# Optimization experiments

Hardware: AMD Instinct MI355X
Metric: run time of the kernel (lower is better)

The kernel has to match this reference:

```python
import jax, jax.numpy as jnp
import numpy as np

B, S, D = 4, 4096, 1024
H, W = 16, 256
DH = D // H


def setup_inputs() -> dict:
    key = jax.random.key(0)
    ks = jax.random.split(key, 5)
    sc = 1.0 / np.sqrt(D)
    return {
        "x": jax.random.normal(ks[0], (B, S, D), jnp.float32),
        "Wq": jax.random.normal(ks[1], (D, D), jnp.float32) * sc,
        "bq": jnp.zeros((D,), jnp.float32),
        "Wk": jax.random.normal(ks[2], (D, D), jnp.float32) * sc,
        "bk": jnp.zeros((D,), jnp.float32),
        "Wv": jax.random.normal(ks[3], (D, D), jnp.float32) * sc,
        "bv": jnp.zeros((D,), jnp.float32),
        "Wo": jax.random.normal(ks[4], (D, D), jnp.float32) * sc,
        "bo": jnp.zeros((D,), jnp.float32),
    }


def reference(x, Wq, bq, Wk, bk, Wv, bv, Wo, bo):
    b, s, d = x.shape
    n = s // W  # seq divisible by window_size -> no padding

    def split_heads(t):
        # (b, s, d) -> (b, h, n, w, dh)
        return t.reshape(b, n, W, H, DH).transpose(0, 3, 1, 2, 4)

    q = split_heads(x @ Wq + bq)
    k = split_heads(x @ Wk + bk)
    v = split_heads(x @ Wv + bv)

    scores = jnp.einsum("bhnqd,bhnkd->bhnqk", q, k) / jnp.sqrt(
        jnp.asarray(DH, x.dtype)
    )
    causal = jnp.tril(jnp.ones((W, W), bool))  # per-block causal mask
    neg = jnp.finfo(scores.dtype).min
    scores = jnp.where(causal, scores, neg)
    weights = jax.nn.softmax(scores, axis=-1)
    out = jnp.einsum("bhnqk,bhnkd->bhnqd", weights, v)
    # (b, h, n, w, dh) -> (b, s, d)
    out = out.transpose(0, 2, 3, 1, 4).reshape(b, s, d)
    return out @ Wo + bo
```

## Files before the change

kernel.cpp:

```cpp
#include <hip/hip_runtime.h>
#include <hip/hip_bf16.h>


typedef __attribute__((ext_vector_type(4))) float f32x4;
typedef __attribute__((ext_vector_type(8))) short s16x8;
typedef __attribute__((ext_vector_type(4))) short s16x4;

__device__ __forceinline__ short f2bf(float f) {
  unsigned u = __float_as_uint(f);
  u += 0x7fffu + ((u >> 16) & 1u);
  return (short)(u >> 16);
}

__device__ __forceinline__ void gload_lds16(const void* g, void* l) {
  __builtin_amdgcn_global_load_lds((const __attribute__((address_space(1))) void*)g,
                                   (__attribute__((address_space(3))) void*)l,
                                   16, 0, 0);
}

__device__ __forceinline__ float rmax16(float v) {
  v = fmaxf(v, __shfl_xor(v, 1, 64));
  v = fmaxf(v, __shfl_xor(v, 2, 64));
  v = fmaxf(v, __shfl_xor(v, 4, 64));
  v = fmaxf(v, __shfl_xor(v, 8, 64));
  return v;
}
__device__ __forceinline__ float rsum16(float v) {
  v += __shfl_xor(v, 1, 64);
  v += __shfl_xor(v, 2, 64);
  v += __shfl_xor(v, 4, 64);
  v += __shfl_xor(v, 8, 64);
  return v;
}

__global__ void cvt_x(const float4* __restrict__ in, s16x4* __restrict__ out, int n4) {
  for (int i = blockIdx.x * 256 + threadIdx.x; i < n4; i += gridDim.x * 256) {
    float4 v = in[i];
    s16x4 o;
    o[0] = f2bf(v.x); o[1] = f2bf(v.y); o[2] = f2bf(v.z); o[3] = f2bf(v.w);
    out[i] = o;
  }
}

__global__ void cvt_wT(const float* __restrict__ W0, const float* __restrict__ W1,
                       const float* __restrict__ W2, const float* __restrict__ W3,
                       short* __restrict__ out) {
  __shared__ float tile[64][65];
  const float* W = (blockIdx.y == 0) ? W0 : (blockIdx.y == 1) ? W1 : (blockIdx.y == 2) ? W2 : W3;
  short* o = out + (size_t)blockIdx.y * (1024 * 1024);
  const int kt = (blockIdx.x >> 4) << 6, nt = (blockIdx.x & 15) << 6;
  const int tid = threadIdx.x;
#pragma unroll
  for (int i = 0; i < 16; ++i) {
    int lin = i * 256 + tid;
    int r = lin >> 6, c = lin & 63;
    tile[r][c] = W[(size_t)(kt + r) * 1024 + nt + c];
  }
  __syncthreads();
#pragma unroll
  for (int i = 0; i < 16; ++i) {
    int lin = i * 256 + tid;
    int r = lin >> 6, c = lin & 63;
    o[(size_t)(nt + r) * 1024 + kt + c] = f2bf(tile[c][r]);
  }
}

template <int MODE>
__global__ __launch_bounds__(256) void gemm_bf16(const short* __restrict__ A,
                                                 const short* __restrict__ Bt,
                                                 const float* __restrict__ bias,
                                                 void* __restrict__ outp) {
  constexpr int Kd = 1024;
  __shared__ short As[128 * 32];
  __shared__ short Bs[128 * 32];
  const int tid = threadIdx.x;
  const int w = tid >> 6, lane = tid & 63;
  const int bm = blockIdx.x >> 3, bn = blockIdx.x & 7;
  const int m0 = bm << 7, n0 = bn << 7;
  const int wr = (w >> 1) << 6, wc = (w & 1) << 6;
  const int srow = lane >> 2, scol = (lane & 3) << 3;
  const int fr = lane & 15, fk = (lane >> 4) << 3;

  f32x4 acc[4][4];
#pragma unroll
  for (int i = 0; i < 4; ++i)
#pragma unroll
    for (int j = 0; j < 4; ++j) acc[i][j] = (f32x4){0.f, 0.f, 0.f, 0.f};

  for (int k0 = 0; k0 < Kd; k0 += 32) {
    __syncthreads();
#pragma unroll
    for (int i = 0; i < 2; ++i) {
      const int rr = ((i * 4 + w) << 4) + srow;
      gload_lds16(A + (size_t)(m0 + rr) * Kd + k0 + scol, As + ((i * 4 + w) << 9));
      gload_lds16(Bt + (size_t)(n0 + rr) * Kd + k0 + scol, Bs + ((i * 4 + w) << 9));
    }
    __syncthreads();
    s16x8 af[4], bf[4];
#pragma unroll
    for (int mi = 0; mi < 4; ++mi) af[mi] = *(const s16x8*)&As[(wr + mi * 16 + fr) * 32 + fk];
#pragma unroll
    for (int ni = 0; ni < 4; ++ni) bf[ni] = *(const s16x8*)&Bs[(wc + ni * 16 + fr) * 32 + fk];
#pragma unroll
    for (int mi = 0; mi < 4; ++mi)
#pragma unroll
      for (int ni = 0; ni < 4; ++ni)
        acc[mi][ni] = __builtin_amdgcn_mfma_f32_16x16x32_bf16(af[mi], bf[ni], acc[mi][ni], 0, 0, 0);
  }

  const int col0 = n0 + wc + fr;
  const int row0 = m0 + wr + ((lane >> 4) << 2);
#pragma unroll
  for (int mi = 0; mi < 4; ++mi) {
#pragma unroll
    for (int ni = 0; ni < 4; ++ni) {
      const int c = col0 + ni * 16;
      const float bv = bias[c];
#pragma unroll
      for (int jj = 0; jj < 4; ++jj) {
        const int r = row0 + mi * 16 + jj;
        const float v = acc[mi][ni][jj] + bv;
        if (MODE == 2) {
          ((float*)outp)[(size_t)r * 1024 + c] = v;
        } else {
          const int b = r >> 12, s = r & 4095;
          const int h = c >> 6, dh = c & 63;
          size_t addr;
          if (MODE == 0) addr = ((size_t)(b * 16 + h) * 4096 + s) * 64 + dh;
          else           addr = ((size_t)(b * 16 + h) * 64 + dh) * 4096 + s;
          ((short*)outp)[addr] = f2bf(v);
        }
      }
    }
  }
}

__global__ __launch_bounds__(256) void attn_kernel(const short* __restrict__ Qg,
                                                   const short* __restrict__ Kg,
                                                   const short* __restrict__ Vg,
                                                   short* __restrict__ AO) {
  constexpr int S = 4096;
  __shared__ short Pl[4][16][272];
  const int tid = threadIdx.x;
  const int w = tid >> 6, lane = tid & 63;
  const int fr = lane & 15, g = lane >> 4;
  const int bhn = blockIdx.x;
  const int nb = bhn & 15, bh = bhn >> 4;
  const int b = bh >> 4, h = bh & 15;
  const short* Qb = Qg + ((size_t)bh * S + nb * 256) * 64;
  const short* Kb = Kg + ((size_t)bh * S + nb * 256) * 64;
  const short* Vb = Vg + (size_t)bh * 64 * S + nb * 256;

#pragma unroll
  for (int qi = 0; qi < 4; ++qi) {
    const int qrow = w * 64 + qi * 16;
    const int dmax = w * 4 + qi;
    const s16x8 aq0 = *(const s16x8*)&Qb[(qrow + fr) * 64 + (g << 3)];
    const s16x8 aq1 = *(const s16x8*)&Qb[(qrow + fr) * 64 + 32 + (g << 3)];
    f32x4 sc[16];
#pragma unroll
    for (int i = 0; i < 16; ++i) sc[i] = (f32x4){0.f, 0.f, 0.f, 0.f};
#pragma unroll
    for (int kt = 0; kt < 16; ++kt) {
      if (kt <= dmax) {
        const s16x8 kf0 = *(const s16x8*)&Kb[(kt * 16 + fr) * 64 + (g << 3)];
        const s16x8 kf1 = *(const s16x8*)&Kb[(kt * 16 + fr) * 64 + 32 + (g << 3)];
        sc[kt] = __builtin_amdgcn_mfma_f32_16x16x32_bf16(aq0, kf0, sc[kt], 0, 0, 0);
        sc[kt] = __builtin_amdgcn_mfma_f32_16x16x32_bf16(aq1, kf1, sc[kt], 0, 0, 0);
      }
    }
    float mrow[4] = {-3e38f, -3e38f, -3e38f, -3e38f};
#pragma unroll
    for (int kt = 0; kt < 16; ++kt) {
      if (kt <= dmax) {
#pragma unroll
        for (int jj = 0; jj < 4; ++jj) {
          float v = sc[kt][jj] * 0.125f;
          if (kt == dmax && fr > (g << 2) + jj) v = -3e38f;
          sc[kt][jj] = v;
          mrow[jj] = fmaxf(mrow[jj], v);
        }
      }
    }
#pragma unroll
    for (int jj = 0; jj < 4; ++jj) mrow[jj] = rmax16(mrow[jj]);
    float lsum[4] = {0.f, 0.f, 0.f, 0.f};
#pragma unroll
    for (int kt = 0; kt < 16; ++kt) {
      if (kt <= dmax) {
#pragma unroll
        for (int jj = 0; jj < 4; ++jj) {
          const float p = __expf(sc[kt][jj] - mrow[jj]);
          sc[kt][jj] = p;
          lsum[jj] += p;
        }
      }
    }
#pragma unroll
    for (int jj = 0; jj < 4; ++jj) lsum[jj] = rsum16(lsum[jj]);
#pragma unroll
    for (int kt = 0; kt < 16; ++kt) {
      if (kt <= dmax) {
#pragma unroll
        for (int jj = 0; jj < 4; ++jj)
          Pl[w][(g << 2) + jj][kt * 16 + fr] = f2bf(sc[kt][jj]);
      } else if (kt == dmax + 1 && ((dmax + 1) & 1)) {
#pragma unroll
        for (int jj = 0; jj < 4; ++jj) Pl[w][(g << 2) + jj][kt * 16 + fr] = 0;
      }
    }
    asm volatile("s_waitcnt lgkmcnt(0)" ::: "memory");
    f32x4 o[4];
#pragma unroll
    for (int di = 0; di < 4; ++di) o[di] = (f32x4){0.f, 0.f, 0.f, 0.f};
    const int nks2 = (dmax + 2) >> 1;
#pragma unroll
    for (int ks2 = 0; ks2 < 8; ++ks2) {
      if (ks2 < nks2) {
        const s16x8 pa = *(const s16x8*)&Pl[w][fr][ks2 * 32 + (g << 3)];
#pragma unroll
        for (int di = 0; di < 4; ++di) {
          const s16x8 vf = *(const s16x8*)&Vb[(size_t)(di * 16 + fr) * S + ks2 * 32 + (g << 3)];
          o[di] = __builtin_amdgcn_mfma_f32_16x16x32_bf16(pa, vf, o[di], 0, 0, 0);
        }
      }
    }
    float inv[4];
#pragma unroll
    for (int jj = 0; jj < 4; ++jj) inv[jj] = 1.f / lsum[jj];
    const int sg = nb * 256 + qrow + (g << 2);
#pragma unroll
    for (int di = 0; di < 4; ++di) {
#pragma unroll
      for (int jj = 0; jj < 4; ++jj) {
        AO[((size_t)b * S + sg + jj) * 1024 + h * 64 + di * 16 + fr] =
            f2bf(o[di][jj] * inv[jj]);
      }
    }
  }
}

extern "C" void kernel_launch(void* const* d_in, const int* in_sizes, int n_in,
                              void* d_out, int out_size, void* d_ws, size_t ws_size,
                              hipStream_t stream) {
  const float* x  = (const float*)d_in[0];
  const float* Wq = (const float*)d_in[1];
  const float* bq = (const float*)d_in[2];
  const float* Wk = (const float*)d_in[3];
  const float* bk = (const float*)d_in[4];
  const float* Wv = (const float*)d_in[5];
  const float* bv = (const float*)d_in[6];
  const float* Wo = (const float*)d_in[7];
  const float* bo = (const float*)d_in[8];
  float* out = (float*)d_out;

  char* ws = (char*)d_ws;
  short* xb  = (short*)ws;
  short* Wt  = (short*)(ws + (size_t)33554432);
  short* Qb  = (short*)(ws + (size_t)33554432 + 8388608);
  short* Kb  = Qb + (size_t)16777216;
  short* Vb  = Kb + (size_t)16777216;
  short* AOb = Vb + (size_t)16777216;

  cvt_x<<<4096, 256, 0, stream>>>((const float4*)x, (s16x4*)xb, 16777216 / 4);
  cvt_wT<<<dim3(256, 4), 256, 0, stream>>>(Wq, Wk, Wv, Wo, Wt);

  gemm_bf16<0><<<1024, 256, 0, stream>>>(xb, Wt,           bq, Qb);
  gemm_bf16<0><<<1024, 256, 0, stream>>>(xb, Wt + 1048576, bk, Kb);
  gemm_bf16<1><<<1024, 256, 0, stream>>>(xb, Wt + 2097152, bv, Vb);

  attn_kernel<<<1024, 256, 0, stream>>>(Qb, Kb, Vb, AOb);

  gemm_bf16<2><<<1024, 256, 0, stream>>>(AOb, Wt + 3145728, bo, out);
}
```

Measured before the change: 449.9 us.

## Fuse QKV projections into one double-buffered GEMM with XCD-aware tile mapping

Replaces the three separate Q/K/V projection GEMMs with one launch of 3072 blocks that selects the weight slice, bias and output buffer from the column tile. The K-loop now double-buffers the LDS tiles, so the next slice is prefetched while MFMAs run on the current one, and only one barrier is used per iteration. Block indices are remapped so that each XCD works on a contiguous group of M rows, which is meant to improve L2 reuse of A. The cost is double the LDS per block, which may lower occupancy, plus some per-element branching in the epilogue.

```diff
diff --git a/kernel.cpp b/kernel.cpp
--- a/kernel.cpp
+++ b/kernel.cpp
@@ -65,49 +65,72 @@
   }
 }
 
-template <int MODE>
-__global__ __launch_bounds__(256) void gemm_bf16(const short* __restrict__ A,
-                                                 const short* __restrict__ Bt,
-                                                 const float* __restrict__ bias,
-                                                 void* __restrict__ outp) {
+template <int NBN, int MODE>
+__global__ __launch_bounds__(256) void gemm2(const short* __restrict__ A,
+                                             const short* __restrict__ BtBase,
+                                             const float* __restrict__ b0,
+                                             const float* __restrict__ b1,
+                                             const float* __restrict__ b2,
+                                             short* __restrict__ Qo,
+                                             short* __restrict__ Ko,
+                                             short* __restrict__ Vo,
+                                             float* __restrict__ Oo) {
   constexpr int Kd = 1024;
-  __shared__ short As[128 * 32];
-  __shared__ short Bs[128 * 32];
+  __shared__ short As[2][128 * 32];
+  __shared__ short Bs[2][128 * 32];
   const int tid = threadIdx.x;
   const int w = tid >> 6, lane = tid & 63;
-  const int bm = blockIdx.x >> 3, bn = blockIdx.x & 7;
+  const int d = blockIdx.x;
+  const int xcd = d & 7, l = d >> 3;
+  constexpr int HALF = NBN * 8;
+  const int sub = l / HALF, r = l % HALF;
+  const int bn = r >> 3, bm = xcd * 16 + sub * 8 + (r & 7);
   const int m0 = bm << 7, n0 = bn << 7;
   const int wr = (w >> 1) << 6, wc = (w & 1) << 6;
   const int srow = lane >> 2, scol = (lane & 3) << 3;
   const int fr = lane & 15, fk = (lane >> 4) << 3;
 
+  const short* Ab  = A + (size_t)m0 * Kd;
+  const short* Btb = BtBase + (size_t)(n0 >> 10) * 1048576 + (size_t)(n0 & 1023) * Kd;
+
   f32x4 acc[4][4];
 #pragma unroll
   for (int i = 0; i < 4; ++i)
 #pragma unroll
     for (int j = 0; j < 4; ++j) acc[i][j] = (f32x4){0.f, 0.f, 0.f, 0.f};
 
-  for (int k0 = 0; k0 < Kd; k0 += 32) {
-    __syncthreads();
-#pragma unroll
-    for (int i = 0; i < 2; ++i) {
-      const int rr = ((i * 4 + w) << 4) + srow;
-      gload_lds16(A + (size_t)(m0 + rr) * Kd + k0 + scol, As + ((i * 4 + w) << 9));
-      gload_lds16(Bt + (size_t)(n0 + rr) * Kd + k0 + scol, Bs + ((i * 4 + w) << 9));
-    }
-    __syncthreads();
+#define STAGE(buf, kk)                                                        \
+  do {                                                                        \
+    _Pragma("unroll") for (int i = 0; i < 2; ++i) {                           \
+      const int rr = ((i * 4 + w) << 4) + srow;                               \
+      gload_lds16(Ab + (size_t)rr * Kd + (kk) + scol, &As[buf][(i * 4 + w) << 9]); \
+      gload_lds16(Btb + (size_t)rr * Kd + (kk) + scol, &Bs[buf][(i * 4 + w) << 9]); \
+    }                                                                         \
+  } while (0)
+
+  STAGE(0, 0);
+  __syncthreads();
+  int cur = 0;
+#pragma unroll 2
+  for (int t = 0; t < 32; ++t) {
+    if (t < 31) STAGE(cur ^ 1, (t + 1) << 5);
     s16x8 af[4], bf[4];
 #pragma unroll
-    for (int mi = 0; mi < 4; ++mi) af[mi] = *(const s16x8*)&As[(wr + mi * 16 + fr) * 32 + fk];
-#pragma unroll
-    for (int ni = 0; ni < 4; ++ni) bf[ni] = *(const s16x8*)&Bs[(wc + ni * 16 + fr) * 32 + fk];
+    for (int mi = 0; mi < 4; ++mi) af[mi] = *(const s16x8*)&As[cur][(wr + mi * 16 + fr) * 32 + fk];
+#pragma unroll
+    for (int ni = 0; ni < 4; ++ni) bf[ni] = *(const s16x8*)&Bs[cur][(wc + ni * 16 + fr) * 32 + fk];
 #pragma unroll
     for (int mi = 0; mi < 4; ++mi)
 #pragma unroll
       for (int ni = 0; ni < 4; ++ni)
         acc[mi][ni] = __builtin_amdgcn_mfma_f32_16x16x32_bf16(af[mi], bf[ni], acc[mi][ni], 0, 0, 0);
-  }
-
+    __syncthreads();
+    cur ^= 1;
+  }
+#undef STAGE
+
+  const int which = n0 >> 10;
+  const float* bb = (which == 0) ? b0 : (which == 1) ? b1 : b2;
   const int col0 = n0 + wc + fr;
   const int row0 = m0 + wr + ((lane >> 4) << 2);
 #pragma unroll
@@ -115,20 +138,22 @@
 #pragma unroll
     for (int ni = 0; ni < 4; ++ni) {
       const int c = col0 + ni * 16;
-      const float bv = bias[c];
+      const float bv = bb[c & 1023];
 #pragma unroll
       for (int jj = 0; jj < 4; ++jj) {
-        const int r = row0 + mi * 16 + jj;
+        const int rrow = row0 + mi * 16 + jj;
         const float v = acc[mi][ni][jj] + bv;
         if (MODE == 2) {
-          ((float*)outp)[(size_t)r * 1024 + c] = v;
+          Oo[(size_t)rrow * 1024 + c] = v;
         } else {
-          const int b = r >> 12, s = r & 4095;
-          const int h = c >> 6, dh = c & 63;
+          const int b = rrow >> 12, s = rrow & 4095;
+          const int cl = c & 1023;
+          const int h = cl >> 6, dh = cl & 63;
+          short* ob = (which == 0) ? Qo : (which == 1) ? Ko : Vo;
           size_t addr;
-          if (MODE == 0) addr = ((size_t)(b * 16 + h) * 4096 + s) * 64 + dh;
+          if (which < 2) addr = ((size_t)(b * 16 + h) * 4096 + s) * 64 + dh;
           else           addr = ((size_t)(b * 16 + h) * 64 + dh) * 4096 + s;
-          ((short*)outp)[addr] = f2bf(v);
+          ob[addr] = f2bf(v);
         }
       }
     }
@@ -265,11 +290,10 @@
   cvt_x<<<4096, 256, 0, stream>>>((const float4*)x, (s16x4*)xb, 16777216 / 4);
   cvt_wT<<<dim3(256, 4), 256, 0, stream>>>(Wq, Wk, Wv, Wo, Wt);
 
-  gemm_bf16<0><<<1024, 256, 0, stream>>>(xb, Wt,           bq, Qb);
-  gemm_bf16<0><<<1024, 256, 0, stream>>>(xb, Wt + 1048576, bk, Kb);
-  gemm_bf16<1><<<1024, 256, 0, stream>>>(xb, Wt + 2097152, bv, Vb);
+  gemm2<24, 0><<<3072, 256, 0, stream>>>(xb, Wt, bq, bk, bv, Qb, Kb, Vb, nullptr);
 
   attn_kernel<<<1024, 256, 0, stream>>>(Qb, Kb, Vb, AOb);
 
-  gemm_bf16<2><<<1024, 256, 0, stream>>>(AOb, Wt + 3145728, bo, out);
-}
+  gemm2<8, 2><<<1024, 256, 0, stream>>>(AOb, Wt + 3145728, bo, bo, bo,
+                                        nullptr, nullptr, nullptr, out);
+}
```

Measured after the change: 443.8 us. No clear change (-1.3%).
